# Kernel optimization log

Hardware: AMD Instinct MI355X
Metric: run time of the kernel (lower is better)

## Reference

```python
import jax, jax.numpy as jnp
import numpy as np

B, SQ, SK, D, H, DH = 4, 1024, 1024, 1024, 16, 64

def setup_inputs() -> dict:
    key = jax.random.key(0)
    ks = jax.random.split(key, 7)
    s = 0.02
    return {
        "input_ids": jax.random.normal(ks[0], (B, SQ, D), jnp.float32),
        "encoder_output": jax.random.normal(ks[1], (B, SK, D), jnp.float32),
        "position_bias": jax.random.normal(ks[2], (1, H, SQ, SK), jnp.float32),
        "Wq": jax.random.normal(ks[3], (D, H * DH), jnp.float32) * s,
        "Wk": jax.random.normal(ks[4], (D, H * DH), jnp.float32) * s,
        "Wv": jax.random.normal(ks[5], (D, H * DH), jnp.float32) * s,
        "Wo": jax.random.normal(ks[6], (H * DH, D), jnp.float32) * s,
    }

def reference(input_ids, encoder_output, position_bias, Wq, Wk, Wv, Wo):
    # bias-free projections (nn.Linear(..., bias=False))
    q = (input_ids @ Wq).reshape(B, SQ, H, DH).transpose(0, 2, 1, 3)      # [B,H,Sq,dh]
    k = (encoder_output @ Wk).reshape(B, SK, H, DH).transpose(0, 2, 1, 3)  # [B,H,Sk,dh]
    v = (encoder_output @ Wv).reshape(B, SK, H, DH).transpose(0, 2, 1, 3)  # [B,H,Sk,dh]
    # T5-style attention: NO 1/sqrt(dh) scaling, additive position bias
    scores = jnp.einsum("bhqd,bhkd->bhqk", q, k) + position_bias          # [B,H,Sq,Sk]
    attn = jax.nn.softmax(scores, axis=-1)
    ctx = jnp.einsum("bhqk,bhkd->bhqd", attn, v)                          # [B,H,Sq,dh]
    ctx = ctx.transpose(0, 2, 1, 3).reshape(B, SQ, H * DH)
    return ctx @ Wo                                                        # [B,Sq,D]
```

## Files before the change

### kernel.cpp

```cpp
#include <hip/hip_runtime.h>

typedef _Float16 f16;
typedef _Float16 f16x4 __attribute__((ext_vector_type(4)));
typedef _Float16 f16x8 __attribute__((ext_vector_type(8)));
typedef float f32x4 __attribute__((ext_vector_type(4)));

#define LOADLDS16(gp, lp)                                                     \
  __builtin_amdgcn_global_load_lds(                                           \
      (const __attribute__((address_space(1))) void*)(gp),                    \
      (__attribute__((address_space(3))) void*)(lp), 16, 0, 0)

__global__ __launch_bounds__(256) void k_cast2(const float* __restrict__ a,
                                               const float* __restrict__ b,
                                               f16* __restrict__ ya,
                                               f16* __restrict__ yb) {
  int i = blockIdx.x * 256 + threadIdx.x;
  const float* x;
  f16* y;
  if (i < 1048576) {
    x = a; y = ya;
  } else {
    x = b; y = yb; i -= 1048576;
  }
  float4 v = reinterpret_cast<const float4*>(x)[i];
  f16x4 o;
  o[0] = (f16)v.x; o[1] = (f16)v.y; o[2] = (f16)v.z; o[3] = (f16)v.w;
  reinterpret_cast<f16x4*>(y)[i] = o;
}

__global__ __launch_bounds__(256) void k_castw_t(
    const float* __restrict__ w0, const float* __restrict__ w1,
    const float* __restrict__ w2, const float* __restrict__ w3,
    f16* __restrict__ o0, f16* __restrict__ o1, f16* __restrict__ o2,
    f16* __restrict__ o3) {
  const float* W;
  f16* O;
  switch (blockIdx.z) {
    case 0: W = w0; O = o0; break;
    case 1: W = w1; O = o1; break;
    case 2: W = w2; O = o2; break;
    default: W = w3; O = o3; break;
  }
  __shared__ f16 T[64][72];
  const int tid = threadIdx.x;
  const int r0 = blockIdx.y * 64, c0 = blockIdx.x * 64;
#pragma unroll
  for (int i = 0; i < 4; ++i) {
    int c = i * 256 + tid;
    int row = c >> 4, col = (c & 15) * 4;
    float4 v = *reinterpret_cast<const float4*>(W + (size_t)(r0 + row) * 1024 + c0 + col);
    T[col + 0][row] = (f16)v.x;
    T[col + 1][row] = (f16)v.y;
    T[col + 2][row] = (f16)v.z;
    T[col + 3][row] = (f16)v.w;
  }
  __syncthreads();
#pragma unroll
  for (int i = 0; i < 2; ++i) {
    int c = i * 256 + tid;
    int cc = c >> 3, ro = (c & 7) * 8;
    f16x8 v;
#pragma unroll
    for (int j = 0; j < 8; ++j) v[j] = T[cc][ro + j];
    *reinterpret_cast<f16x8*>(O + (size_t)(c0 + cc) * 1024 + r0 + ro) = v;
  }
}

__global__ __launch_bounds__(256) void k_gemm_qkv(const f16* __restrict__ Xq,
                                                  const f16* __restrict__ Xkv,
                                                  const f16* __restrict__ Bt,
                                                  f16* __restrict__ outp) {
  __shared__ f16 As[128 * 64];
  __shared__ f16 Bs[128 * 64];
  const int tid = threadIdx.x;
  const int w = tid >> 6, l = tid & 63;
  const int lr = l & 15, lq = l >> 4;
  const int m0 = blockIdx.y * 128, n0 = blockIdx.x * 128;
  const f16* A = (n0 < 1024) ? Xq : Xkv;
  const int wr = (w >> 1) * 64, wc = (w & 1) * 64;
  const int K = 1024;
  f32x4 acc[4][4] = {};
  for (int kt = 0; kt < K; kt += 64) {
#pragma unroll
    for (int i = 0; i < 4; ++i) {
      int c = (i * 4 + w) * 64 + l;
      LOADLDS16(A + (size_t)(m0 + (c >> 3)) * K + kt + (c & 7) * 8,
                As + (size_t)(i * 4 + w) * 512);
      LOADLDS16(Bt + (size_t)(n0 + (c >> 3)) * K + kt + (c & 7) * 8,
                Bs + (size_t)(i * 4 + w) * 512);
    }
    __syncthreads();
#pragma unroll
    for (int kk = 0; kk < 2; ++kk) {
      f16x8 af[4], bf[4];
#pragma unroll
      for (int m = 0; m < 4; ++m)
        af[m] = *reinterpret_cast<const f16x8*>(As + (wr + m * 16 + lr) * 64 + kk * 32 + lq * 8);
#pragma unroll
      for (int n = 0; n < 4; ++n)
        bf[n] = *reinterpret_cast<const f16x8*>(Bs + (wc + n * 16 + lr) * 64 + kk * 32 + lq * 8);
#pragma unroll
      for (int m = 0; m < 4; ++m)
#pragma unroll
        for (int n = 0; n < 4; ++n)
          acc[m][n] = __builtin_amdgcn_mfma_f32_16x16x32_f16(af[m], bf[n], acc[m][n], 0, 0, 0);
    }
    __syncthreads();
  }
#pragma unroll
  for (int m = 0; m < 4; ++m)
#pragma unroll
    for (int n = 0; n < 4; ++n)
#pragma unroll
      for (int r = 0; r < 4; ++r) {
        int row = m0 + wr + m * 16 + lq * 4 + r;
        int col = n0 + wc + n * 16 + lr;
        int b = row >> 10, s = row & 1023;
        int plane = col >> 10, cc = col & 1023;
        int h = cc >> 6, dh = cc & 63;
        outp[(size_t)plane * 4194304 +
             (((size_t)(b * 16 + h)) * 1024 + s) * 64 + dh] = (f16)acc[m][n][r];
      }
}

__global__ __launch_bounds__(256) void k_gemm_o(const f16* __restrict__ A,
                                                const f16* __restrict__ Bt,
                                                float* __restrict__ out, int M,
                                                int N, int K) {
  __shared__ f16 As[64 * 64];
  __shared__ f16 Bs[128 * 64];
  const int tid = threadIdx.x;
  const int w = tid >> 6, l = tid & 63;
  const int lr = l & 15, lq = l >> 4;
  const int m0 = blockIdx.y * 64, n0 = blockIdx.x * 128;
  const int wr = (w >> 1) * 32, wc = (w & 1) * 64;
  f32x4 acc[2][4] = {};
  for (int kt = 0; kt < K; kt += 64) {
#pragma unroll
    for (int i = 0; i < 2; ++i) {
      int c = (i * 4 + w) * 64 + l;
      LOADLDS16(A + (size_t)(m0 + (c >> 3)) * K + kt + (c & 7) * 8,
                As + (size_t)(i * 4 + w) * 512);
    }
#pragma unroll
    for (int i = 0; i < 4; ++i) {
      int c = (i * 4 + w) * 64 + l;
      LOADLDS16(Bt + (size_t)(n0 + (c >> 3)) * K + kt + (c & 7) * 8,
                Bs + (size_t)(i * 4 + w) * 512);
    }
    __syncthreads();
#pragma unroll
    for (int kk = 0; kk < 2; ++kk) {
      f16x8 af[2], bf[4];
#pragma unroll
      for (int m = 0; m < 2; ++m)
        af[m] = *reinterpret_cast<const f16x8*>(As + (wr + m * 16 + lr) * 64 + kk * 32 + lq * 8);
#pragma unroll
      for (int n = 0; n < 4; ++n)
        bf[n] = *reinterpret_cast<const f16x8*>(Bs + (wc + n * 16 + lr) * 64 + kk * 32 + lq * 8);
#pragma unroll
      for (int m = 0; m < 2; ++m)
#pragma unroll
        for (int n = 0; n < 4; ++n)
          acc[m][n] = __builtin_amdgcn_mfma_f32_16x16x32_f16(af[m], bf[n], acc[m][n], 0, 0, 0);
    }
    __syncthreads();
  }
#pragma unroll
  for (int m = 0; m < 2; ++m)
#pragma unroll
    for (int n = 0; n < 4; ++n)
#pragma unroll
      for (int r = 0; r < 4; ++r) {
        int row = m0 + wr + m * 16 + lq * 4 + r;
        int col = n0 + wc + n * 16 + lr;
        out[(size_t)row * N + col] = acc[m][n][r];
      }
}

__global__ __launch_bounds__(256) void k_vtrans(const f16* __restrict__ vb,
                                                f16* __restrict__ vtb) {
  const int bh = blockIdx.y, s0 = blockIdx.x * 64;
  __shared__ f16 T[64][72];
  const int tid = threadIdx.x;
  const f16* src = vb + (size_t)bh * 1024 * 64;
#pragma unroll
  for (int i = 0; i < 2; ++i) {
    int c = i * 256 + tid;
    int row = c >> 3, co = (c & 7) * 8;
    f16x8 v = *reinterpret_cast<const f16x8*>(src + (size_t)(s0 + row) * 64 + co);
#pragma unroll
    for (int j = 0; j < 8; ++j) T[co + j][row] = v[j];
  }
  __syncthreads();
  f16* dst = vtb + (size_t)bh * 64 * 1024;
#pragma unroll
  for (int i = 0; i < 2; ++i) {
    int c = i * 256 + tid;
    int dh = c >> 3, so = (c & 7) * 8;
    f16x8 v;
#pragma unroll
    for (int j = 0; j < 8; ++j) v[j] = T[dh][so + j];
    *reinterpret_cast<f16x8*>(dst + (size_t)dh * 1024 + s0 + so) = v;
  }
}

__global__ __launch_bounds__(256, 2) void k_attn(const f16* __restrict__ qb,
                                                 const f16* __restrict__ kb,
                                                 const f16* __restrict__ vtb,
                                                 const float* __restrict__ bias,
                                                 f16* __restrict__ ctx) {
  const int bid = blockIdx.x;
  const int ord = (bid & 7) * 64 + (bid >> 3);
  const int h = ord >> 5, qt = (ord >> 2) & 7, b = ord & 3;
  const int bh = b * 16 + h;
  const int q0 = qt * 128;
  const int tid = threadIdx.x, w = tid >> 6, l = tid & 63;
  const int lr = l & 15, lq = l >> 4;

  __shared__ f16 Kb3[3][2048];
  __shared__ f16 Vb3[3][2048];
  __shared__ float Bb2[2][4096];
  __shared__ f16 Ps[4][1280];

  const f16* qp = qb + ((size_t)bh * 1024 + q0 + w * 32 + lr) * 64 + lq * 8;
  f16x8 qA0 = *reinterpret_cast<const f16x8*>(qp);
  f16x8 qA1 = *reinterpret_cast<const f16x8*>(qp + 32);
  f16x8 qB0 = *reinterpret_cast<const f16x8*>(qp + 1024);
  f16x8 qB1 = *reinterpret_cast<const f16x8*>(qp + 1056);

  f32x4 OA[4] = {}, OB[4] = {};
  float mA = -3.0e38f, mB = -3.0e38f, rsA = 0.f, rsB = 0.f;

  const f16* kbase = kb + (size_t)bh * 65536;
  const f16* vbase = vtb + (size_t)bh * 65536;
  const float* bbase = bias + ((size_t)h * 1024 + q0) * 1024;

  const int krow = w * 8 + (l >> 3), kg = (l & 7) ^ (l >> 3);
  const int vrow = w * 16 + (l >> 2), vg = (l & 3) ^ ((l >> 3) & 3);

  auto stage_kv = [&](int t, int c3) {
    LOADLDS16(kbase + (size_t)(t * 32 + krow) * 64 + kg * 8, &Kb3[c3][w * 512]);
    LOADLDS16(vbase + (size_t)vrow * 1024 + t * 32 + vg * 8, &Vb3[c3][w * 512]);
  };
  auto stage_b = [&](int t, int c2) {
#pragma unroll
    for (int j = 0; j < 4; ++j) {
      int c4 = w * 4 + j;
      int row = c4 * 8 + (l >> 3);
      int gs = (l & 7) ^ (l >> 3);
      LOADLDS16(bbase + (size_t)row * 1024 + t * 32 + gs * 4,
                &Bb2[c2][c4 * 256]);
    }
  };

  stage_b(0, 0);
  stage_kv(0, 0);
  stage_kv(1, 1);

#pragma unroll 1
  for (int t = 0; t < 32; ++t) {
    if (t < 31) {
      asm volatile("s_waitcnt vmcnt(2)" ::: "memory");
    } else {
      asm volatile("s_waitcnt vmcnt(0)" ::: "memory");
    }
    __builtin_amdgcn_s_barrier();
    __builtin_amdgcn_sched_barrier(0);

    if (t + 1 < 32) stage_b(t + 1, (t + 1) & 1);
    if (t + 2 < 32) stage_kv(t + 2, (t + 2) % 3);
    __builtin_amdgcn_sched_barrier(0);

    const int c3 = t % 3, c2 = t & 1;
    const f16* Kc = &Kb3[c3][0];
    const f16* Vc = &Vb3[c3][0];
    const float* Bc = &Bb2[c2][0];

    f32x4 S[2][2];
#pragma unroll
    for (int f = 0; f < 2; ++f)
#pragma unroll
      for (int c = 0; c < 2; ++c) {
        int row = w * 32 + f * 16 + lr;
        int pos = (c * 4 + lq) ^ (lr & 7);
        S[f][c] = *reinterpret_cast<const f32x4*>(&Bc[row * 32 + pos * 4]);
      }

    __builtin_amdgcn_s_setprio(1);
#pragma unroll
    for (int c = 0; c < 2; ++c) {
      int row = c * 16 + lr;
      const f16* kbp = &Kc[row * 64];
      f16x8 kf0 = *reinterpret_cast<const f16x8*>(kbp + ((lq ^ (lr & 7)) * 8));
      f16x8 kf1 = *reinterpret_cast<const f16x8*>(kbp + (((4 + lq) ^ (lr & 7)) * 8));
      S[0][c] = __builtin_amdgcn_mfma_f32_16x16x32_f16(kf0, qA0, S[0][c], 0, 0, 0);
      S[0][c] = __builtin_amdgcn_mfma_f32_16x16x32_f16(kf1, qA1, S[0][c], 0, 0, 0);
      S[1][c] = __builtin_amdgcn_mfma_f32_16x16x32_f16(kf0, qB0, S[1][c], 0, 0, 0);
      S[1][c] = __builtin_amdgcn_mfma_f32_16x16x32_f16(kf1, qB1, S[1][c], 0, 0, 0);
    }
    __builtin_amdgcn_s_setprio(0);

    float tA = fmaxf(fmaxf(fmaxf(S[0][0][0], S[0][0][1]), fmaxf(S[0][0][2], S[0][0][3])),
                     fmaxf(fmaxf(S[0][1][0], S[0][1][1]), fmaxf(S[0][1][2], S[0][1][3])));
    float tB = fmaxf(fmaxf(fmaxf(S[1][0][0], S[1][0][1]), fmaxf(S[1][0][2], S[1][0][3])),
                     fmaxf(fmaxf(S[1][1][0], S[1][1][1]), fmaxf(S[1][1][2], S[1][1][3])));
    bool ok = (tA <= mA + 8.0f) && (tB <= mB + 8.0f);
    if (!__all(ok)) {
      tA = fmaxf(tA, __shfl_xor(tA, 16, 64));
      tA = fmaxf(tA, __shfl_xor(tA, 32, 64));
      tB = fmaxf(tB, __shfl_xor(tB, 16, 64));
      tB = fmaxf(tB, __shfl_xor(tB, 32, 64));
      float mnA = fmaxf(mA, tA), mnB = fmaxf(mB, tB);
      float scA = __expf(mA - mnA), scB = __expf(mB - mnB);
      mA = mnA; mB = mnB;
      rsA *= scA; rsB *= scB;
      int sb = l & 48;
#pragma unroll
      for (int r = 0; r < 4; ++r) {
        float sA = __shfl(scA, sb | (lq * 4 + r), 64);
        float sB = __shfl(scB, sb | (lq * 4 + r), 64);
#pragma unroll
        for (int c = 0; c < 4; ++c) {
          OA[c][r] *= sA;
          OB[c][r] *= sB;
        }
      }
    }

#pragma unroll
    for (int c = 0; c < 2; ++c) {
      f32x4 pA, pB;
#pragma unroll
      for (int r = 0; r < 4; ++r) {
        pA[r] = __expf(S[0][c][r] - mA);
        pB[r] = __expf(S[1][c][r] - mB);
      }
      rsA += (pA[0] + pA[1]) + (pA[2] + pA[3]);
      rsB += (pB[0] + pB[1]) + (pB[2] + pB[3]);
      f16x4 hA = {(f16)pA[0], (f16)pA[1], (f16)pA[2], (f16)pA[3]};
      f16x4 hB = {(f16)pB[0], (f16)pB[1], (f16)pB[2], (f16)pB[3]};
      *reinterpret_cast<f16x4*>(&Ps[w][lr * 40 + c * 16 + lq * 4]) = hA;
      *reinterpret_cast<f16x4*>(&Ps[w][(16 + lr) * 40 + c * 16 + lq * 4]) = hB;
    }

    {
      f16x8 paA = *reinterpret_cast<const f16x8*>(&Ps[w][lr * 40 + lq * 8]);
      f16x8 paB = *reinterpret_cast<const f16x8*>(&Ps[w][(16 + lr) * 40 + lq * 8]);
      __builtin_amdgcn_s_setprio(1);
#pragma unroll
      for (int c = 0; c < 4; ++c) {
        int row = c * 16 + lr;
        f16x8 vf = *reinterpret_cast<const f16x8*>(
            &Vc[row * 32 + ((lq ^ ((lr >> 1) & 3)) * 8)]);
        OA[c] = __builtin_amdgcn_mfma_f32_16x16x32_f16(paA, vf, OA[c], 0, 0, 0);
        OB[c] = __builtin_amdgcn_mfma_f32_16x16x32_f16(paB, vf, OB[c], 0, 0, 0);
      }
      __builtin_amdgcn_s_setprio(0);
    }
  }

  rsA += __shfl_xor(rsA, 16, 64);
  rsA += __shfl_xor(rsA, 32, 64);
  rsB += __shfl_xor(rsB, 16, 64);
  rsB += __shfl_xor(rsB, 32, 64);
  int sb = l & 48;

#pragma unroll
  for (int r = 0; r < 4; ++r) {
    float dA = __shfl(rsA, sb | (lq * 4 + r), 64);
    float dB = __shfl(rsB, sb | (lq * 4 + r), 64);
    int rowA = q0 + w * 32 + lq * 4 + r;
#pragma unroll
    for (int c = 0; c < 4; ++c) {
      int col = h * 64 + c * 16 + lr;
      ctx[((size_t)b * 1024 + rowA) * 1024 + col] = (f16)(OA[c][r] / dA);
      ctx[((size_t)b * 1024 + rowA + 16) * 1024 + col] = (f16)(OB[c][r] / dB);
    }
  }
}

extern "C" void kernel_launch(void* const* d_in, const int* in_sizes, int n_in,
                              void* d_out, int out_size, void* d_ws,
                              size_t ws_size, hipStream_t stream) {
  const float* input_ids = (const float*)d_in[0];
  const float* enc = (const float*)d_in[1];
  const float* bias = (const float*)d_in[2];
  const float* Wq = (const float*)d_in[3];
  const float* Wk = (const float*)d_in[4];
  const float* Wv = (const float*)d_in[5];
  const float* Wo = (const float*)d_in[6];

  char* ws = (char*)d_ws;
  const size_t MB = 1024 * 1024;
  f16* Xq  = (f16*)(ws + 0 * MB);
  f16* Xkv = (f16*)(ws + 8 * MB);
  f16* Wqt = (f16*)(ws + 16 * MB);
  f16* Wkt = (f16*)(ws + 18 * MB);
  f16* Wvt = (f16*)(ws + 20 * MB);
  f16* Wot = (f16*)(ws + 22 * MB);
  f16* qbuf = (f16*)(ws + 24 * MB);
  f16* kbuf = (f16*)(ws + 32 * MB);
  f16* vbuf = (f16*)(ws + 40 * MB);
  f16* vtb = Xkv;
  f16* ctxb = Xq;

  k_cast2<<<8192, 256, 0, stream>>>(input_ids, enc, Xq, Xkv);
  k_castw_t<<<dim3(16, 16, 4), 256, 0, stream>>>(Wq, Wk, Wv, Wo, Wqt, Wkt, Wvt, Wot);

  k_gemm_qkv<<<dim3(24, 32), 256, 0, stream>>>(Xq, Xkv, Wqt, qbuf);

  k_vtrans<<<dim3(16, 64), 256, 0, stream>>>(vbuf, vtb);

  k_attn<<<512, 256, 0, stream>>>(qbuf, kbuf, vtb, bias, ctxb);

  k_gemm_o<<<dim3(8, 64), 256, 0, stream>>>(ctxb, Wot, (float*)d_out, 4096, 1024, 1024);
}
```

Before: 140.3 us.

## Load position bias directly into registers, bypassing LDS staging

The position-bias tile is no longer staged through a double-buffered LDS array with global_load_lds. Each lane now loads its own bias fragments straight from global memory into registers one tile ahead, using a ping-pong register pair and a loop unrolled by two. The bias is added after the QK MFMAs instead of being used as the accumulator's initial value. This frees 32KB of LDS and removes the LDS read traffic for bias. In exchange it adds VGPR pressure and makes the global bias loads less coalesced (16-byte reads per lane along rows), and the vmcnt waits are retuned to match.

Measured after the change: 141.8 us. About the same (+1.0%).

```diff
diff --git a/kernel.cpp b/kernel.cpp
--- a/kernel.cpp
+++ b/kernel.cpp
@@ -220,7 +220,6 @@
 
   __shared__ f16 Kb3[3][2048];
   __shared__ f16 Vb3[3][2048];
-  __shared__ float Bb2[2][4096];
   __shared__ f16 Ps[4][1280];
 
   const f16* qp = qb + ((size_t)bh * 1024 + q0 + w * 32 + lr) * 64 + lq * 8;
@@ -234,7 +233,9 @@
 
   const f16* kbase = kb + (size_t)bh * 65536;
   const f16* vbase = vtb + (size_t)bh * 65536;
-  const float* bbase = bias + ((size_t)h * 1024 + q0) * 1024;
+  const float* bq0 =
+      bias + ((size_t)h * 1024 + q0 + w * 32 + lr) * 1024 + lq * 4;
+  const float* bq1 = bq0 + 16 * 1024;
 
   const int krow = w * 8 + (l >> 3), kg = (l & 7) ^ (l >> 3);
   const int vrow = w * 16 + (l >> 2), vg = (l & 3) ^ ((l >> 3) & 3);
@@ -243,50 +244,42 @@
     LOADLDS16(kbase + (size_t)(t * 32 + krow) * 64 + kg * 8, &Kb3[c3][w * 512]);
     LOADLDS16(vbase + (size_t)vrow * 1024 + t * 32 + vg * 8, &Vb3[c3][w * 512]);
   };
-  auto stage_b = [&](int t, int c2) {
-#pragma unroll
-    for (int j = 0; j < 4; ++j) {
-      int c4 = w * 4 + j;
-      int row = c4 * 8 + (l >> 3);
-      int gs = (l & 7) ^ (l >> 3);
-      LOADLDS16(bbase + (size_t)row * 1024 + t * 32 + gs * 4,
-                &Bb2[c2][c4 * 256]);
-    }
-  };
-
-  stage_b(0, 0);
+
   stage_kv(0, 0);
   stage_kv(1, 1);
-
-#pragma unroll 1
-  for (int t = 0; t < 32; ++t) {
-    if (t < 31) {
-      asm volatile("s_waitcnt vmcnt(2)" ::: "memory");
+  f32x4 bcA[2][2], bcB[2][2];
+#pragma unroll
+  for (int c = 0; c < 2; ++c) {
+    bcA[0][c] = *reinterpret_cast<const f32x4*>(bq0 + c * 16);
+    bcA[1][c] = *reinterpret_cast<const f32x4*>(bq1 + c * 16);
+  }
+
+  auto body = [&](int t, f32x4 (&bc)[2][2], f32x4 (&bn)[2][2]) {
+    if (t == 31) {
+      asm volatile("s_waitcnt vmcnt(4)" ::: "memory");
     } else {
-      asm volatile("s_waitcnt vmcnt(0)" ::: "memory");
+      asm volatile("s_waitcnt vmcnt(6)" ::: "memory");
     }
     __builtin_amdgcn_s_barrier();
     __builtin_amdgcn_sched_barrier(0);
 
-    if (t + 1 < 32) stage_b(t + 1, (t + 1) & 1);
+    if (t + 1 < 32) {
+      const float* b0 = bq0 + (t + 1) * 32;
+      const float* b1 = bq1 + (t + 1) * 32;
+#pragma unroll
+      for (int c = 0; c < 2; ++c) {
+        bn[0][c] = *reinterpret_cast<const f32x4*>(b0 + c * 16);
+        bn[1][c] = *reinterpret_cast<const f32x4*>(b1 + c * 16);
+      }
+    }
     if (t + 2 < 32) stage_kv(t + 2, (t + 2) % 3);
     __builtin_amdgcn_sched_barrier(0);
 
-    const int c3 = t % 3, c2 = t & 1;
+    const int c3 = t % 3;
     const f16* Kc = &Kb3[c3][0];
     const f16* Vc = &Vb3[c3][0];
-    const float* Bc = &Bb2[c2][0];
-
-    f32x4 S[2][2];
-#pragma unroll
-    for (int f = 0; f < 2; ++f)
-#pragma unroll
-      for (int c = 0; c < 2; ++c) {
-        int row = w * 32 + f * 16 + lr;
-        int pos = (c * 4 + lq) ^ (lr & 7);
-        S[f][c] = *reinterpret_cast<const f32x4*>(&Bc[row * 32 + pos * 4]);
-      }
-
+
+    f32x4 S[2][2] = {};
     __builtin_amdgcn_s_setprio(1);
 #pragma unroll
     for (int c = 0; c < 2; ++c) {
@@ -300,6 +293,13 @@
       S[1][c] = __builtin_amdgcn_mfma_f32_16x16x32_f16(kf1, qB1, S[1][c], 0, 0, 0);
     }
     __builtin_amdgcn_s_setprio(0);
+
+#pragma unroll
+    for (int f = 0; f < 2; ++f)
+#pragma unroll
+      for (int c = 0; c < 2; ++c)
+#pragma unroll
+        for (int r = 0; r < 4; ++r) S[f][c][r] += bc[f][c][r];
 
     float tA = fmaxf(fmaxf(fmaxf(S[0][0][0], S[0][0][1]), fmaxf(S[0][0][2], S[0][0][3])),
                      fmaxf(fmaxf(S[0][1][0], S[0][1][1]), fmaxf(S[0][1][2], S[0][1][3])));
@@ -358,6 +358,12 @@
       }
       __builtin_amdgcn_s_setprio(0);
     }
+  };
+
+#pragma unroll 1
+  for (int ith = 0; ith < 16; ++ith) {
+    body(2 * ith, bcA, bcB);
+    body(2 * ith + 1, bcB, bcA);
   }
 
   rsA += __shfl_xor(rsA, 16, 64);
```
